# Performance work log

Measured on AMD Instinct MI355X. Metric: run time of the kernel, lower is better.

The kernel has to match this reference:

```python
import jax, jax.numpy as jnp
import numpy as np

N = 4096
SPECIES = 100
FEA = 64        # atom_emb_dim
NBR_FEA = 64    # num gaussians
MAX_NBRS = 12
LN_EPS = 1e-5

# GaussianSmearing constants: linspace(0, 8, 64)
_OFFSET = jnp.linspace(0.0, 8.0, NBR_FEA)
_COEFF = -0.5 / float(8.0 / (NBR_FEA - 1)) ** 2


def _uniform(key, shape, fan_in):
    s = 1.0 / np.sqrt(fan_in)
    return jax.random.uniform(key, shape, minval=-s, maxval=s, dtype=jnp.float32)


def setup_inputs() -> dict:
    key = jax.random.key(0)
    ks = jax.random.split(key, 20)
    lat_pred = jnp.eye(3, dtype=jnp.float32) * 8.0 + 0.2 * jax.random.normal(ks[0], (3, 3), dtype=jnp.float32)
    fracs_pred = jax.random.uniform(ks[1], (N, 3), dtype=jnp.float32)
    species_logits = jax.random.normal(ks[2], (N, SPECIES), dtype=jnp.float32)
    occ_logits = jax.random.normal(ks[3], (N,), dtype=jnp.float32)
    # params
    emb_w = _uniform(ks[4], (SPECIES, FEA), SPECIES)
    emb_b = _uniform(ks[5], (FEA,), SPECIES)
    in1 = 2 * FEA + NBR_FEA  # 192
    w1 = _uniform(ks[6], (in1, 2 * FEA), in1)
    b1 = _uniform(ks[7], (2 * FEA,), in1)
    g1 = jnp.ones((2 * FEA,), jnp.float32)
    be1 = jnp.zeros((2 * FEA,), jnp.float32)
    w2 = _uniform(ks[8], (in1, 2 * FEA), in1)
    b2 = _uniform(ks[9], (2 * FEA,), in1)
    g2 = jnp.ones((2 * FEA,), jnp.float32)
    be2 = jnp.zeros((2 * FEA,), jnp.float32)
    fc_w = _uniform(ks[10], (FEA, 1), FEA)
    fc_b = _uniform(ks[11], (1,), FEA)
    return dict(lat_pred=lat_pred, fracs_pred=fracs_pred, species_logits=species_logits,
                occ_logits=occ_logits, emb_w=emb_w, emb_b=emb_b,
                w1=w1, b1=b1, g1=g1, be1=be1, w2=w2, b2=b2, g2=g2, be2=be2,
                fc_w=fc_w, fc_b=fc_b)


def _layernorm(x, g, b):
    m = jnp.mean(x, axis=-1, keepdims=True)
    v = jnp.var(x, axis=-1, keepdims=True)
    return (x - m) * jax.lax.rsqrt(v + LN_EPS) * g + b


def _cgcnn_layer(atom, nbr_atom, nbr_fea, w, b, g, be):
    # atom: [N,F]; nbr_atom: [N,M,F]; nbr_fea: [N,M,K]
    n, m = nbr_atom.shape[:2]
    atom_exp = jnp.broadcast_to(atom[:, None, :], (n, m, atom.shape[-1]))
    total = jnp.concatenate([atom_exp, nbr_atom, nbr_fea], axis=2)  # [N,M,2F+K]
    z = _layernorm(total @ w + b, g, be)                            # [N,M,2F]
    nbr_filter, nbr_core = jnp.split(z, 2, axis=2)
    nbr_sumed = jnp.sum(jax.nn.sigmoid(nbr_filter) * jax.nn.softplus(nbr_core), axis=1)
    return jax.nn.softplus(atom + nbr_sumed)


def reference(lat_pred, fracs_pred, species_logits, occ_logits,
              emb_w, emb_b, w1, b1, g1, be1, w2, b2, g2, be2, fc_w, fc_b):
    species_probs = jax.nn.softmax(species_logits, axis=-1)
    atom_fea = species_probs @ emb_w + emb_b                         # [N,F]
    diff = fracs_pred[:, None, :] - fracs_pred[None, :, :]           # [N,N,3]
    diff = diff - jnp.round(diff)                                    # min-image
    cart = diff @ lat_pred                                           # [N,N,3]
    dist = jnp.linalg.norm(cart, axis=-1)                            # [N,N]
    dist = dist + jnp.eye(dist.shape[0], dtype=dist.dtype) * 100.0
    k = min(MAX_NBRS, dist.shape[1] - 1)
    neg_d, nbr_idx = jax.lax.top_k(-dist, k)                         # smallest k
    nbr_dist = -neg_d                                                # [N,k]
    nbr_fea = jnp.exp(_COEFF * (nbr_dist[..., None] - _OFFSET) ** 2) # [N,k,K]
    nbr_atom_fea = atom_fea[nbr_idx]                                 # [N,k,F]
    atom_fea = _cgcnn_layer(atom_fea, nbr_atom_fea, nbr_fea, w1, b1, g1, be1)
    atom_fea = _cgcnn_layer(atom_fea, nbr_atom_fea, nbr_fea, w2, b2, g2, be2)
    occ_probs = jax.nn.sigmoid(occ_logits)[:, None]                  # [N,1]
    graph_fea = jnp.sum(atom_fea * occ_probs, axis=0) / (jnp.sum(occ_probs) + 1e-6)
    return graph_fea @ fc_w + fc_b                                   # [1]
```

## Files before the change

### kernel.cpp

```cpp
#include <hip/hip_runtime.h>
#include <math.h>

#define N_ATOMS 4096
#define SPECIES 100
#define FEA 64
#define M_NBR 12

typedef unsigned short u16;
typedef __attribute__((ext_vector_type(8))) _Float16 f16x8;
typedef __attribute__((ext_vector_type(4))) float f32x4;

constexpr float LN_EPS = 1e-5f;
constexpr float GAUSS_COEFF = -31.0078125f;
constexpr float D2_INF = 3.4e38f;

__device__ __forceinline__ float sigmoidf_(float x){
    return __fdividef(1.0f, 1.0f + __expf(-x));
}
__device__ __forceinline__ float softplusf_(float x){
    return fmaxf(x, 0.0f) + __logf(1.0f + __expf(-fabsf(x)));
}
__device__ __forceinline__ u16 f16bits(_Float16 h){ return *(u16*)&h; }

__global__ __launch_bounds__(256) void k_setup(const float* __restrict__ fracs,
        const float* __restrict__ w1, const float* __restrict__ w2,
        const float* __restrict__ logits, const float* __restrict__ emb_w,
        const float* __restrict__ emb_b,
        float* __restrict__ fx, float* __restrict__ fy, float* __restrict__ fz,
        u16* __restrict__ wpk, float* __restrict__ atom0, u16* __restrict__ a0f){
    __shared__ float sE[4][SPECIES];
    int b = blockIdx.x, t = threadIdx.x;
    if (b < 192){
        int gid = b * 256 + t;
        int layer = gid / 24576;
        int e = gid % 24576;
        int k = e >> 7, n = e & 127;
        float x = (layer ? w2 : w1)[e];
        int mat = layer * 3 + (k >> 6);
        int kk = k & 63;
        int ch = kk >> 5, lg2 = (kk >> 3) & 3, i = kk & 7;
        int nt = n >> 4, lr2 = n & 15;
        wpk[mat * 8192 + ((ch * 8 + nt) * 64 + (lg2 * 16 + lr2)) * 8 + i] = f16bits((_Float16)x);
    } else if (b < 208){
        int j = (b - 192) * 256 + t;
        fx[j] = fracs[j*3+0];
        fy[j] = fracs[j*3+1];
        fz[j] = fracs[j*3+2];
    } else {
        int grp = t >> 6, f = t & 63;
        int a = (b - 208) * 4 + grp;
        const float* lg = logits + (long)a * SPECIES;
        float l0 = lg[f];
        float l1 = (f + 64 < SPECIES) ? lg[f + 64] : -1e30f;
        float mx = fmaxf(l0, l1);
        #pragma unroll
        for (int off = 32; off; off >>= 1) mx = fmaxf(mx, __shfl_xor(mx, off));
        float e0 = __expf(l0 - mx);
        float e1 = (f + 64 < SPECIES) ? __expf(l1 - mx) : 0.0f;
        sE[grp][f] = e0;
        if (f + 64 < SPECIES) sE[grp][64 + f] = e1;
        float sm = e0 + e1;
        #pragma unroll
        for (int off = 32; off; off >>= 1) sm += __shfl_xor(sm, off);
        __syncthreads();
        float acc = 0.0f;
        for (int s = 0; s < SPECIES; ++s) acc += sE[grp][s] * emb_w[s * FEA + f];
        float v = acc / sm + emb_b[f];
        atom0[(long)a * FEA + f] = v;
        a0f[a * FEA + f] = f16bits((_Float16)v);
    }
}

__global__ __launch_bounds__(256) void k_topk(const float* __restrict__ fx,
        const float* __restrict__ fy, const float* __restrict__ fz,
        const float* __restrict__ lat, int* __restrict__ nbr_idx,
        float* __restrict__ nbr_dist){
    __shared__ int   hist[256];
    __shared__ int   cnt;
    __shared__ float sThr;
    __shared__ float candD[256];
    __shared__ int   candI[256];
    int i = blockIdx.x, tid = threadIdx.x;
    hist[tid] = 0;
    if (tid == 0) cnt = 0;
    __syncthreads();
    float l00=lat[0],l01=lat[1],l02=lat[2];
    float l10=lat[3],l11=lat[4],l12=lat[5];
    float l20=lat[6],l21=lat[7],l22=lat[8];
    float xi = fx[i], yi = fy[i], zi = fz[i];
    float d2r[16];
    #pragma unroll
    for (int k = 0; k < 16; ++k){
        int j = tid + k * 256;
        float dx = xi - fx[j];
        float dy = yi - fy[j];
        float dz = zi - fz[j];
        dx -= rintf(dx); dy -= rintf(dy); dz -= rintf(dz);
        float cx = dx*l00 + dy*l10 + dz*l20;
        float cy = dx*l01 + dy*l11 + dz*l21;
        float cz = dx*l02 + dy*l12 + dz*l22;
        float d2 = cx*cx + cy*cy + cz*cz;
        if (j == i) d2 = D2_INF;
        d2r[k] = d2;
        if (d2 < 4.0f) atomicAdd(&hist[(int)(d2 * 64.0f)], 1);
    }
    __syncthreads();
    if (tid < 64){
        int s0 = hist[4*tid] + hist[4*tid+1] + hist[4*tid+2] + hist[4*tid+3];
        int sc = s0;
        #pragma unroll
        for (int off = 1; off < 64; off <<= 1){
            int o = __shfl_up(sc, off);
            if (tid >= off) sc += o;
        }
        unsigned long long mball = __ballot(sc >= M_NBR);
        if (mball == 0ULL){
            if (tid == 0) sThr = 1e30f;
        } else {
            int gbin = __ffsll(mball) - 1;
            if (tid == gbin){
                int c = sc - s0;
                float th = 4.0f;
                #pragma unroll
                for (int b = 0; b < 4; ++b){
                    c += hist[4*gbin + b];
                    if (c >= M_NBR){ th = (float)(4*gbin + b + 1) * (1.0f/64.0f); break; }
                }
                sThr = th;
            }
        }
    }
    __syncthreads();
    float thr = sThr;
    #pragma unroll
    for (int k = 0; k < 16; ++k){
        if (d2r[k] < thr){
            int p = atomicAdd(&cnt, 1);
            if (p < 256){ candD[p] = d2r[k]; candI[p] = tid + k * 256; }
        }
    }
    __syncthreads();
    int n = cnt < 256 ? cnt : 256;
    for (int c = tid; c < n; c += 256){
        float dv = candD[c]; int iv = candI[c];
        int rank = 0;
        for (int s = 0; s < n; ++s){
            float ds_ = candD[s]; int is_ = candI[s];
            rank += (ds_ < dv || (ds_ == dv && is_ < iv)) ? 1 : 0;
        }
        if (rank < M_NBR){
            nbr_idx[i * M_NBR + rank]  = iv;
            nbr_dist[i * M_NBR + rank] = sqrtf(dv);
        }
    }
}

__global__ __launch_bounds__(64, 4) void k_atom(
        const float* __restrict__ atom0F, const u16* __restrict__ a0f,
        const int* __restrict__ nbr_idx, const float* __restrict__ nbr_dist,
        const u16* __restrict__ wpk,
        const float* __restrict__ b1, const float* __restrict__ g1, const float* __restrict__ be1,
        const float* __restrict__ b2, const float* __restrict__ g2, const float* __restrict__ be2,
        float* __restrict__ outF)
{
    __shared__ u16   sH[64];
    __shared__ float sO[64];

    const int a = blockIdx.x;
    const int l = threadIdx.x;
    const int lg = l >> 4, lr = l & 15;

    const int slot = (lr < 12) ? lr : 11;
    const int nid  = nbr_idx[a * M_NBR + slot];
    const float dist = nbr_dist[a * M_NBR + slot];
    f16x8 nfr[2], saf[2];
    nfr[0] = *(const f16x8*)(a0f + nid * 64 + lg * 8);
    nfr[1] = *(const f16x8*)(a0f + nid * 64 + 32 + lg * 8);
    saf[0] = *(const f16x8*)(a0f + a * 64 + lg * 8);
    saf[1] = *(const f16x8*)(a0f + a * 64 + 32 + lg * 8);
    float resv[4];
    #pragma unroll
    for (int nt = 0; nt < 4; ++nt)
        resv[nt] = atom0F[(long)a * 64 + nt * 16 + lr];

    f16x8 ga[2];
    #pragma unroll
    for (int c = 0; c < 2; ++c)
        #pragma unroll
        for (int i = 0; i < 8; ++i){
            int k = c * 32 + lg * 8 + i;
            float dd = dist - (float)k * (8.0f / 63.0f);
            ga[c][i] = (_Float16)__expf(GAUSS_COEFF * dd * dd);
        }

    #pragma unroll 1
    for (int layer = 0; layer < 2; ++layer){
        const u16* wb = wpk + layer * 3 * 8192;
        const float* bb  = layer ? b2  : b1;
        const float* gg  = layer ? g2  : g1;
        const float* bee = layer ? be2 : be1;

        f32x4 acc[8];
        #pragma unroll
        for (int nt = 0; nt < 8; ++nt) acc[nt] = 0.0f;
        #pragma unroll
        for (int c = 0; c < 2; ++c)
            #pragma unroll
            for (int nt = 0; nt < 8; ++nt){
                const f16x8 bS = *(const f16x8*)(wb +          ((c * 8 + nt) * 64 + l) * 8);
                const f16x8 bN = *(const f16x8*)(wb +  8192 + ((c * 8 + nt) * 64 + l) * 8);
                const f16x8 bG = *(const f16x8*)(wb + 16384 + ((c * 8 + nt) * 64 + l) * 8);
                acc[nt] = __builtin_amdgcn_mfma_f32_16x16x32_f16(saf[c], bS, acc[nt], 0, 0, 0);
                acc[nt] = __builtin_amdgcn_mfma_f32_16x16x32_f16(nfr[c], bN, acc[nt], 0, 0, 0);
                acc[nt] = __builtin_amdgcn_mfma_f32_16x16x32_f16(ga[c],  bG, acc[nt], 0, 0, 0);
            }

        float s[4] = {0,0,0,0}, q[4] = {0,0,0,0};
        #pragma unroll
        for (int nt = 0; nt < 8; ++nt){
            float bv = bb[nt * 16 + lr];
            #pragma unroll
            for (int rr = 0; rr < 4; ++rr){
                float v = acc[nt][rr] + bv;
                acc[nt][rr] = v;
                s[rr] += v; q[rr] += v * v;
            }
        }
        #pragma unroll
        for (int rr = 0; rr < 4; ++rr){
            #pragma unroll
            for (int m = 1; m < 16; m <<= 1){
                s[rr] += __shfl_xor(s[rr], m);
                q[rr] += __shfl_xor(q[rr], m);
            }
        }
        float nsum[4];
        #pragma unroll
        for (int nt = 0; nt < 4; ++nt){
            float gf = gg[nt * 16 + lr],      bef = bee[nt * 16 + lr];
            float gc = gg[64 + nt * 16 + lr], bec = bee[64 + nt * 16 + lr];
            float part = 0.0f;
            #pragma unroll
            for (int rr = 0; rr < 4; ++rr){
                float mean = s[rr] * (1.0f / 128.0f);
                float var  = q[rr] * (1.0f / 128.0f) - mean * mean;
                float inv  = rsqrtf(var + LN_EPS);
                float zf = (acc[nt][rr]     - mean) * inv * gf + bef;
                float zc = (acc[nt + 4][rr] - mean) * inv * gc + bec;
                part += sigmoidf_(zf) * softplusf_(zc);
            }
            if (lg == 3) part = 0.0f;
            part += __shfl_xor(part, 16);
            part += __shfl_xor(part, 32);
            nsum[nt] = part;
        }
        #pragma unroll
        for (int nt = 0; nt < 4; ++nt)
            resv[nt] = softplusf_(resv[nt] + nsum[nt]);

        if (layer == 0){
            if (lg == 0){
                #pragma unroll
                for (int nt = 0; nt < 4; ++nt)
                    sH[nt * 16 + lr] = f16bits((_Float16)resv[nt]);
            }
            __syncthreads();
            saf[0] = *(const f16x8*)(&sH[lg * 8]);
            saf[1] = *(const f16x8*)(&sH[32 + lg * 8]);
        } else {
            if (lg == 0){
                #pragma unroll
                for (int nt = 0; nt < 4; ++nt)
                    sO[nt * 16 + lr] = resv[nt];
            }
            __syncthreads();
            outF[(long)a * 64 + l] = sO[l];
        }
    }
}

__global__ __launch_bounds__(256) void k_partial(const float* __restrict__ atom,
        const float* __restrict__ occ, float* __restrict__ partials){
    int b = blockIdx.x, tid = threadIdx.x;
    int f = tid & 63, sub = tid >> 6;
    __shared__ float sAcc[256];
    float acc = 0.0f;
    for (int it = 0; it < 16; ++it){
        int a = b * 64 + sub + it * 4;
        float p = sigmoidf_(occ[a]);
        acc += atom[(long)a * FEA + f] * p;
    }
    sAcc[tid] = acc;
    __syncthreads();
    if (tid < 64){
        float s = sAcc[f] + sAcc[64 + f] + sAcc[128 + f] + sAcc[192 + f];
        partials[b * 65 + f] = s;
        float po = sigmoidf_(occ[b * 64 + f]);
        #pragma unroll
        for (int off = 32; off; off >>= 1) po += __shfl_down(po, off);
        if (f == 0) partials[b * 65 + 64] = po;
    }
}

__global__ __launch_bounds__(64) void k_final(const float* __restrict__ partials,
        const float* __restrict__ fc_w, const float* __restrict__ fc_b,
        float* __restrict__ out){
    int f = threadIdx.x;
    float num = 0.0f;
    for (int p = 0; p < 64; ++p) num += partials[p * 65 + f];
    float occs = partials[f * 65 + 64];
    #pragma unroll
    for (int off = 32; off; off >>= 1) occs += __shfl_down(occs, off);
    occs = __shfl(occs, 0);
    float gf = num / (occs + 1e-6f);
    float v = gf * fc_w[f];
    #pragma unroll
    for (int off = 32; off; off >>= 1) v += __shfl_down(v, off);
    if (f == 0) out[0] = v + fc_b[0];
}

extern "C" void kernel_launch(void* const* d_in, const int* in_sizes, int n_in,
                              void* d_out, int out_size, void* d_ws, size_t ws_size,
                              hipStream_t stream) {
    const float* lat    = (const float*)d_in[0];
    const float* fracs  = (const float*)d_in[1];
    const float* slog   = (const float*)d_in[2];
    const float* occ    = (const float*)d_in[3];
    const float* emb_w  = (const float*)d_in[4];
    const float* emb_b  = (const float*)d_in[5];
    const float* w1     = (const float*)d_in[6];
    const float* b1     = (const float*)d_in[7];
    const float* g1     = (const float*)d_in[8];
    const float* be1    = (const float*)d_in[9];
    const float* w2     = (const float*)d_in[10];
    const float* b2     = (const float*)d_in[11];
    const float* g2     = (const float*)d_in[12];
    const float* be2    = (const float*)d_in[13];
    const float* fc_w   = (const float*)d_in[14];
    const float* fc_b   = (const float*)d_in[15];
    float* out = (float*)d_out;

    char* ws = (char*)d_ws;
    auto alloc = [&](size_t bytes) -> void* {
        void* p = (void*)ws;
        ws += (bytes + 255) & ~(size_t)255;
        return p;
    };
    int*   nbr_idx  = (int*)  alloc((size_t)N_ATOMS * M_NBR * 4);
    float* nbr_dist = (float*)alloc((size_t)N_ATOMS * M_NBR * 4);
    float* atom0    = (float*)alloc((size_t)N_ATOMS * FEA * 4);
    float* atom1    = (float*)alloc((size_t)N_ATOMS * FEA * 4);
    u16*   a0f      = (u16*)  alloc((size_t)N_ATOMS * FEA * 2);
    u16*   wpk      = (u16*)  alloc((size_t)6 * 8192 * 2);
    float* fxa      = (float*)alloc((size_t)N_ATOMS * 4);
    float* fya      = (float*)alloc((size_t)N_ATOMS * 4);
    float* fza      = (float*)alloc((size_t)N_ATOMS * 4);
    float* partials = (float*)alloc((size_t)64 * 65 * 4);

    k_setup  <<<208 + N_ATOMS / 4, 256, 0, stream>>>(fracs, w1, w2, slog, emb_w, emb_b,
                fxa, fya, fza, wpk, atom0, a0f);
    k_topk   <<<N_ATOMS, 256, 0, stream>>>(fxa, fya, fza, lat, nbr_idx, nbr_dist);
    k_atom   <<<N_ATOMS, 64, 0, stream>>>(atom0, a0f, nbr_idx, nbr_dist,
                wpk, b1, g1, be1, b2, g2, be2, atom1);
    k_partial<<<64, 256, 0, stream>>>(atom1, occ, partials);
    k_final  <<<1, 64, 0, stream>>>(partials, fc_w, fc_b, out);
}
```

Before: 61.85 us.

## Stage weights in LDS and process four atoms per block in k_atom

```diff
diff --git a/kernel.cpp b/kernel.cpp
--- a/kernel.cpp
+++ b/kernel.cpp
@@ -155,7 +155,7 @@
     }
 }
 
-__global__ __launch_bounds__(64, 4) void k_atom(
+__global__ __launch_bounds__(256) void k_atom(
         const float* __restrict__ atom0F, const u16* __restrict__ a0f,
         const int* __restrict__ nbr_idx, const float* __restrict__ nbr_dist,
         const u16* __restrict__ wpk,
@@ -163,12 +163,21 @@
         const float* __restrict__ b2, const float* __restrict__ g2, const float* __restrict__ be2,
         float* __restrict__ outF)
 {
-    __shared__ u16   sH[64];
-    __shared__ float sO[64];
-
-    const int a = blockIdx.x;
-    const int l = threadIdx.x;
+    __shared__ u16   wlds[24576];
+    __shared__ u16   sH[4][64];
+    __shared__ float sO[4][64];
+
+    const int t = threadIdx.x;
+    const int w = t >> 6, l = t & 63;
     const int lg = l >> 4, lr = l & 15;
+    const int a = blockIdx.x * 4 + w;
+
+    {
+        const float4* wsrc = (const float4*)wpk;
+        #pragma unroll
+        for (int it = 0; it < 12; ++it)
+            ((float4*)wlds)[it * 256 + t] = wsrc[it * 256 + t];
+    }
 
     const int slot = (lr < 12) ? lr : 11;
     const int nid  = nbr_idx[a * M_NBR + slot];
@@ -193,9 +202,10 @@
             ga[c][i] = (_Float16)__expf(GAUSS_COEFF * dd * dd);
         }
 
+    __syncthreads();
+
     #pragma unroll 1
     for (int layer = 0; layer < 2; ++layer){
-        const u16* wb = wpk + layer * 3 * 8192;
         const float* bb  = layer ? b2  : b1;
         const float* gg  = layer ? g2  : g1;
         const float* bee = layer ? be2 : be1;
@@ -207,9 +217,9 @@
         for (int c = 0; c < 2; ++c)
             #pragma unroll
             for (int nt = 0; nt < 8; ++nt){
-                const f16x8 bS = *(const f16x8*)(wb +          ((c * 8 + nt) * 64 + l) * 8);
-                const f16x8 bN = *(const f16x8*)(wb +  8192 + ((c * 8 + nt) * 64 + l) * 8);
-                const f16x8 bG = *(const f16x8*)(wb + 16384 + ((c * 8 + nt) * 64 + l) * 8);
+                const f16x8 bS = *(const f16x8*)(&wlds[         ((c * 8 + nt) * 64 + l) * 8]);
+                const f16x8 bN = *(const f16x8*)(&wlds[ 8192 + ((c * 8 + nt) * 64 + l) * 8]);
+                const f16x8 bG = *(const f16x8*)(&wlds[16384 + ((c * 8 + nt) * 64 + l) * 8]);
                 acc[nt] = __builtin_amdgcn_mfma_f32_16x16x32_f16(saf[c], bS, acc[nt], 0, 0, 0);
                 acc[nt] = __builtin_amdgcn_mfma_f32_16x16x32_f16(nfr[c], bN, acc[nt], 0, 0, 0);
                 acc[nt] = __builtin_amdgcn_mfma_f32_16x16x32_f16(ga[c],  bG, acc[nt], 0, 0, 0);
@@ -262,19 +272,25 @@
             if (lg == 0){
                 #pragma unroll
                 for (int nt = 0; nt < 4; ++nt)
-                    sH[nt * 16 + lr] = f16bits((_Float16)resv[nt]);
-            }
+                    sH[w][nt * 16 + lr] = f16bits((_Float16)resv[nt]);
+            }
+            saf[0] = *(const f16x8*)(&sH[w][lg * 8]);
+            saf[1] = *(const f16x8*)(&sH[w][32 + lg * 8]);
             __syncthreads();
-            saf[0] = *(const f16x8*)(&sH[lg * 8]);
-            saf[1] = *(const f16x8*)(&sH[32 + lg * 8]);
+            {
+                const float4* wsrc2 = (const float4*)(wpk + 3 * 8192);
+                #pragma unroll
+                for (int it = 0; it < 12; ++it)
+                    ((float4*)wlds)[it * 256 + t] = wsrc2[it * 256 + t];
+            }
+            __syncthreads();
         } else {
             if (lg == 0){
                 #pragma unroll
                 for (int nt = 0; nt < 4; ++nt)
-                    sO[nt * 16 + lr] = resv[nt];
-            }
-            __syncthreads();
-            outF[(long)a * 64 + l] = sO[l];
+                    sO[w][nt * 16 + lr] = resv[nt];
+            }
+            outF[(long)a * 64 + l] = sO[w][l];
         }
     }
 }
@@ -360,7 +376,7 @@
     k_setup  <<<208 + N_ATOMS / 4, 256, 0, stream>>>(fracs, w1, w2, slog, emb_w, emb_b,
                 fxa, fya, fza, wpk, atom0, a0f);
     k_topk   <<<N_ATOMS, 256, 0, stream>>>(fxa, fya, fza, lat, nbr_idx, nbr_dist);
-    k_atom   <<<N_ATOMS, 64, 0, stream>>>(atom0, a0f, nbr_idx, nbr_dist,
+    k_atom   <<<N_ATOMS / 4, 256, 0, stream>>>(atom0, a0f, nbr_idx, nbr_dist,
                 wpk, b1, g1, be1, b2, g2, be2, atom1);
     k_partial<<<64, 256, 0, stream>>>(atom1, occ, partials);
     k_final  <<<1, 64, 0, stream>>>(partials, fc_w, fc_b, out);
```

Result: faster. 58.91 us (-4.8%).
